# Kernel optimization log

Measured on AMD Instinct MI355X. Metric: run time of the kernel, lower is better.

Reference implementation:

```python
import jax, jax.numpy as jnp
import numpy as np

K, D = 512, 256

def setup_inputs() -> dict:
    key = jax.random.key(0)
    k1, k2 = jax.random.split(key)
    z_e = jax.random.normal(k1, (64, D, 32, 32), dtype=jnp.float32)
    # matches nn.Embedding weight init uniform_(-1/K, 1/K)
    codebook = jax.random.uniform(k2, (K, D), dtype=jnp.float32, minval=-1.0 / K, maxval=1.0 / K)
    return {"z_e": z_e, "codebook": codebook}

def reference(z_e, codebook):
    N, Dd, H, W = z_e.shape
    # NCHW -> (N*H*W, D) tokens
    x = jnp.transpose(z_e, (0, 2, 3, 1)).reshape(-1, Dd)
    x_sq = jnp.sum(x * x, axis=1, keepdims=True)            # [T, 1]
    w_sq = jnp.sum(codebook * codebook, axis=1)             # [K]
    dists = x_sq - 2.0 * (x @ codebook.T) + w_sq[None, :]   # [T, K]
    q = jnp.argmin(dists, axis=1)                           # [T]
    z_q = codebook[q]                                       # [T, D] gather
    z_q = z_q.reshape(N, H, W, Dd).transpose(0, 3, 1, 2)    # back to NCHW
    q = q.reshape(N, H, W).astype(jnp.int64)
    return (q, z_q)
```

## Files before the change

### kernel.cpp

```cpp
#include <hip/hip_runtime.h>
#include <float.h>
#include <math.h>


#define KCODES 512
#define DDIM   256
#define HWSZ   1024
#define TTOK   65536
#define TPB    64
#define NBLK   (TTOK / TPB)
#define NCHUNK 16
#define MARGIN 2.5e-4f

#define HW_OFF 66560
#define BK_OFF 68608
#define LDS_SZ 68864
#define ZQ_PITCH 1040

typedef short bf16x8 __attribute__((ext_vector_type(8)));
typedef float f32x16 __attribute__((ext_vector_type(16)));
typedef float f32x4  __attribute__((ext_vector_type(4)));

__device__ inline unsigned short bf16rne(float x) {
    union { float f; unsigned u; } a; a.f = x;
    unsigned r = a.u + (0x7fffu + ((a.u >> 16) & 1u));
    return (unsigned short)(r >> 16);
}
__device__ inline float bf16tof(unsigned short h) {
    union { unsigned u; float f; } b; b.u = ((unsigned)h) << 16; return b.f;
}

__device__ __forceinline__ void top4_insert(float m, int c, float fb[4], int fi[4]) {
    #pragma unroll
    for (int l = 0; l < 4; ++l) {
        const bool s = m > fb[l];
        const float nm = s ? fb[l] : m;
        const int   nc = s ? fi[l] : c;
        fb[l] = s ? m : fb[l];
        fi[l] = s ? c : fi[l];
        m = nm; c = nc;
    }
}

__global__ __launch_bounds__(256) void vq_wsq_np(const float* __restrict__ cb,
                                                 float* __restrict__ wsq) {
    const int tid = threadIdx.x;
    const int k = blockIdx.x * 16 + (tid >> 4);
    const int s = tid & 15, h2 = s >> 3, j2 = s & 7;
    const float* p = cb + (size_t)k * DDIM + h2 * 128 + j2;
    float v[16];
    #pragma unroll
    for (int i = 0; i < 16; ++i) v[i] = p[i * 8];
    float rr;
    {
#pragma clang fp contract(off)
        rr = v[0] * v[0];
        #pragma unroll
        for (int i = 1; i < 16; ++i) { float sq = v[i] * v[i]; rr = rr + sq; }
    }
    float t = rr;
    t = t + __shfl_xor(t, 1);
    t = t + __shfl_xor(t, 2);
    t = t + __shfl_xor(t, 4);
    t = t + __shfl_xor(t, 8);
    if (s == 0) wsq[k] = t;
}

__global__ __launch_bounds__(256) void vq_wpack(const float* __restrict__ cb,
                                                unsigned char* __restrict__ wsw) {
    const int gid = blockIdx.x * 256 + threadIdx.x;
    const int k = gid >> 5, o = gid & 31;
    const int d0 = o * 8, c = o >> 1, half = o & 1;
    unsigned hi[4], lo[4];
    #pragma unroll
    for (int jj = 0; jj < 4; ++jj) {
        float v0 = cb[k * DDIM + d0 + 2 * jj];
        float v1 = cb[k * DDIM + d0 + 2 * jj + 1];
        unsigned short h0 = bf16rne(v0), h1 = bf16rne(v1);
        unsigned short l0 = bf16rne(v0 - bf16tof(h0));
        unsigned short l1 = bf16rne(v1 - bf16tof(h1));
        hi[jj] = (unsigned)h0 | ((unsigned)h1 << 16);
        lo[jj] = (unsigned)l0 | ((unsigned)l1 << 16);
    }
    const int tile = k >> 5, lane2 = (k & 31) + 32 * half;
    *(uint4*)(wsw + ((size_t)((c * 2 + 0) * 16 + tile) * 1024) + lane2 * 16) = make_uint4(hi[0], hi[1], hi[2], hi[3]);
    *(uint4*)(wsw + ((size_t)((c * 2 + 1) * 16 + tile) * 1024) + lane2 * 16) = make_uint4(lo[0], lo[1], lo[2], lo[3]);
}

__global__ __launch_bounds__(512, 4) void vq_main(const float* __restrict__ z_e,
                                                  const float* __restrict__ cb,
                                                  const float* __restrict__ wsq,
                                                  const unsigned char* __restrict__ wsw,
                                                  float* __restrict__ out) {
    __shared__ __align__(16) unsigned char lds[LDS_SZ];

    const int tid = threadIdx.x;
    const int wv = tid >> 6, lane = tid & 63;
    const int tbase = blockIdx.x * TPB;
    const int n = tbase >> 10, hw0 = tbase & (HWSZ - 1);
    const float* zb = z_e + (size_t)n * (DDIM * HWSZ) + hw0;

    {
        const int tok = tid & 63, g = tid >> 6;
        const int mtS = tok >> 5;
        const int lbase = (tok & 31) * 16;
        #pragma unroll
        for (int o = 0; o < 4; ++o) {
            const int d0 = g * 32 + o * 8;
            float v[8];
            #pragma unroll
            for (int j = 0; j < 8; ++j) v[j] = zb[(size_t)(d0 + j) * HWSZ + tok];
            unsigned hi[4], lo[4];
            #pragma unroll
            for (int jj = 0; jj < 4; ++jj) {
                unsigned short h0 = bf16rne(v[2 * jj]), h1 = bf16rne(v[2 * jj + 1]);
                unsigned short l0 = bf16rne(v[2 * jj] - bf16tof(h0));
                unsigned short l1 = bf16rne(v[2 * jj + 1] - bf16tof(h1));
                hi[jj] = (unsigned)h0 | ((unsigned)h1 << 16);
                lo[jj] = (unsigned)l0 | ((unsigned)l1 << 16);
            }
            const int c = d0 >> 4;
            const int off2 = lbase + 512 * ((d0 >> 3) & 1);
            *(uint4*)(lds + ((0 * 2 + mtS) * 16 + c) * 1024 + off2) = make_uint4(hi[0], hi[1], hi[2], hi[3]);
            *(uint4*)(lds + ((1 * 2 + mtS) * 16 + c) * 1024 + off2) = make_uint4(lo[0], lo[1], lo[2], lo[3]);
        }
    }
    ((float*)(lds + HW_OFF))[tid] = 0.5f * wsq[tid];

    __syncthreads();

    const int qc = wv >> 1;
    const int mt = wv & 1;
    const int hh = lane >> 5;
    const float* hwsqL = (const float*)(lds + HW_OFF);

    #define LDW(c, p, t)   (*(const bf16x8*)(wsw + ((size_t)(((c) * 2 + (p)) * 16 + (t)) * 1024) + lane * 16))
    #define LDA(p, mm, c)  (*(const bf16x8*)(lds + (((p) * 2 + (mm)) * 16 + (c)) * 1024 + lane * 16))

    float fb[4] = {-FLT_MAX, -FLT_MAX, -FLT_MAX, -FLT_MAX};
    int   fi[4] = {KCODES, KCODES, KCODES, KCODES};

    #pragma unroll
    for (int pr = 0; pr < 2; ++pr) {
        const int ct0 = qc * 4 + 2 * pr;
        f32x16 a0, a1;
        #pragma unroll
        for (int r = 0; r < 16; ++r) { a0[r] = 0.f; a1[r] = 0.f; }
        bf16x8 Xc[2][2], Wc[2][4];
        Xc[0][0] = LDA(0, mt, 0);  Xc[0][1] = LDA(1, mt, 0);
        Wc[0][0] = LDW(0, 0, ct0); Wc[0][1] = LDW(0, 1, ct0);
        Wc[0][2] = LDW(0, 0, ct0 + 1); Wc[0][3] = LDW(0, 1, ct0 + 1);
        #pragma unroll
        for (int c = 0; c < NCHUNK; ++c) {
            const int cur = c & 1, nxt = cur ^ 1;
            if (c + 1 < NCHUNK) {
                Xc[nxt][0] = LDA(0, mt, c + 1);  Xc[nxt][1] = LDA(1, mt, c + 1);
                Wc[nxt][0] = LDW(c + 1, 0, ct0); Wc[nxt][1] = LDW(c + 1, 1, ct0);
                Wc[nxt][2] = LDW(c + 1, 0, ct0 + 1); Wc[nxt][3] = LDW(c + 1, 1, ct0 + 1);
            }
            a0 = __builtin_amdgcn_mfma_f32_32x32x16_bf16(Wc[cur][0], Xc[cur][0], a0, 0, 0, 0);
            a1 = __builtin_amdgcn_mfma_f32_32x32x16_bf16(Wc[cur][2], Xc[cur][0], a1, 0, 0, 0);
            a0 = __builtin_amdgcn_mfma_f32_32x32x16_bf16(Wc[cur][1], Xc[cur][0], a0, 0, 0, 0);
            a1 = __builtin_amdgcn_mfma_f32_32x32x16_bf16(Wc[cur][3], Xc[cur][0], a1, 0, 0, 0);
            a0 = __builtin_amdgcn_mfma_f32_32x32x16_bf16(Wc[cur][0], Xc[cur][1], a0, 0, 0, 0);
            a1 = __builtin_amdgcn_mfma_f32_32x32x16_bf16(Wc[cur][2], Xc[cur][1], a1, 0, 0, 0);
        }
        #pragma unroll
        for (int rq = 0; rq < 4; ++rq) {
            const f32x4 h40 = *(const f32x4*)(hwsqL + ct0 * 32 + rq * 8 + 4 * hh);
            const f32x4 h41 = *(const f32x4*)(hwsqL + (ct0 + 1) * 32 + rq * 8 + 4 * hh);
            #pragma unroll
            for (int rr = 0; rr < 4; ++rr) {
                top4_insert(a0[rq * 4 + rr] - h40[rr], ct0 * 32 + rr + 8 * rq + 4 * hh, fb, fi);
                top4_insert(a1[rq * 4 + rr] - h41[rr], (ct0 + 1) * 32 + rr + 8 * rq + 4 * hh, fb, fi);
            }
        }
    }

    {
        float sb[4]; int si[4];
        #pragma unroll
        for (int c = 0; c < 4; ++c) { sb[c] = __shfl_xor(fb[c], 32); si[c] = __shfl_xor(fi[c], 32); }
        #pragma unroll
        for (int c = 0; c < 4; ++c) top4_insert(sb[c], si[c], fb, fi);
    }

    __syncthreads();
    float* candm = (float*)lds;
    int*   candi = (int*)(lds + 4096);
    int*   wlCnt = (int*)(lds + 8192);
    int*   wlTok = (int*)(lds + 8208);
    int*   wlGi  = (int*)(lds + 8464);
    float* wlG   = (float*)(lds + 9488);
    int*   bkArr = (int*)(lds + BK_OFF);
    if (lane < 32) {
        const int slot = (qc * 64 + mt * 32 + lane) * 4;
        #pragma unroll
        for (int c = 0; c < 4; ++c) { candm[slot + c] = fb[c]; candi[slot + c] = fi[c]; }
    }
    if (tid == 0) *wlCnt = 0;
    __syncthreads();

    if (tid < TPB) {
        float g[4] = {-FLT_MAX, -FLT_MAX, -FLT_MAX, -FLT_MAX};
        int  gi[4] = {KCODES, KCODES, KCODES, KCODES};
        #pragma unroll
        for (int q4 = 0; q4 < 4; ++q4) {
            const int slot = (q4 * 64 + tid) * 4;
            #pragma unroll
            for (int c = 0; c < 4; ++c) top4_insert(candm[slot + c], candi[slot + c], g, gi);
        }
        if (g[0] - g[1] > MARGIN) {
            out[tbase + tid] = (float)gi[0];
            bkArr[tid] = gi[0];
        } else {
            const int slot = atomicAdd(wlCnt, 1);
            wlTok[slot] = tid;
            #pragma unroll
            for (int c = 0; c < 4; ++c) { wlGi[slot * 4 + c] = gi[c]; wlG[slot * 4 + c] = g[c]; }
        }
    }
    __syncthreads();

    {
        const int nIt = *wlCnt;
        for (int it = wv; it < nIt; it += 8) {
            const int tok = wlTok[it];
            const float g0 = wlG[it * 4];
            const float* xa = zb + tok;

            float xsq;
            {
                const int h2 = (lane >> 3) & 1, j2 = lane & 7;
                float v[16];
                if (lane < 16) {
                    #pragma unroll
                    for (int i = 0; i < 16; ++i)
                        v[i] = xa[(size_t)(h2 * 128 + i * 8 + j2) * HWSZ];
                } else {
                    #pragma unroll
                    for (int i = 0; i < 16; ++i) v[i] = 0.f;
                }
                float rr;
                {
#pragma clang fp contract(off)
                    rr = v[0] * v[0];
                    #pragma unroll
                    for (int i = 1; i < 16; ++i) { float sq = v[i] * v[i]; rr = rr + sq; }
                }
                float t = rr;
                t = t + __shfl_xor(t, 1);
                t = t + __shfl_xor(t, 2);
                t = t + __shfl_xor(t, 4);
                t = t + __shfl_xor(t, 8);
                xsq = __shfl(t, 0);
            }

            double xv[4];
            #pragma unroll
            for (int i = 0; i < 4; ++i)
                xv[i] = (double)xa[(size_t)(lane + 64 * i) * HWSZ];

            float bestd = FLT_MAX; int bestk = KCODES;
            #pragma unroll
            for (int c = 0; c < 4; ++c) {
                const float gc = wlG[it * 4 + c];
                if (c > 0 && g0 - gc > MARGIN) break;
                const int idx = wlGi[it * 4 + c];
                const float* wr = cb + (size_t)idx * DDIM;
                double A = 0.0;
                #pragma unroll
                for (int i = 0; i < 4; ++i)
                    A = fma((double)wr[lane + 64 * i], xv[i], A);
                A = A + __shfl_xor(A, 1);
                A = A + __shfl_xor(A, 2);
                A = A + __shfl_xor(A, 4);
                A = A + __shfl_xor(A, 8);
                A = A + __shfl_xor(A, 16);
                A = A + __shfl_xor(A, 32);
                float dist;
                {
#pragma clang fp contract(off)
                    const float xw = (float)A;
                    const float t1 = xsq - 2.0f * xw;
                    dist = t1 + wsq[idx];
                }
                if (dist < bestd || (dist == bestd && idx < bestk)) { bestd = dist; bestk = idx; }
            }
            if (lane == 0) {
                out[tbase + tok] = (float)bestk;
                bkArr[tok] = bestk;
            }
        }
    }
    __syncthreads();

    {
        #pragma unroll
        for (int rr = 0; rr < 8; ++rr) {
            const int r = wv * 8 + rr;
            const int bk = bkArr[r];
            const float4 vv = *(const float4*)(cb + (size_t)bk * DDIM + lane * 4);
            *(float4*)(lds + r * ZQ_PITCH + lane * 16) = vv;
        }
    }
    __syncthreads();

    {
        const int tk = tid & 63, s = tid >> 6;
        float* zq = out + TTOK + (size_t)n * (DDIM * HWSZ) + hw0 + tk;
        #pragma unroll
        for (int i = 0; i < 32; i += 4) {
            const f32x4 v = *(const f32x4*)(lds + tk * ZQ_PITCH + (s * 32 + i) * 4);
            #pragma unroll
            for (int j = 0; j < 4; ++j)
                zq[(size_t)(s * 32 + i + j) * HWSZ] = v[j];
        }
    }
}

extern "C" void kernel_launch(void* const* d_in, const int* in_sizes, int n_in,
                              void* d_out, int out_size, void* d_ws, size_t ws_size,
                              hipStream_t stream) {
    const float* z_e = (const float*)d_in[0];
    const float* cb  = (const float*)d_in[1];
    float* out = (float*)d_out;
    float* wsq = (float*)d_ws;
    unsigned char* wsw = (unsigned char*)d_ws + 2048;

    vq_wsq_np<<<32, 256, 0, stream>>>(cb, wsq);
    vq_wpack<<<64, 256, 0, stream>>>(cb, wsw);
    vq_main<<<NBLK, 512, 0, stream>>>(z_e, cb, wsq, wsw, out);
}
```

Before: 184.2 us.

## Halve tokens per block to 32 and merge codebook prep kernels

Each block in the main kernel now handles 32 tokens instead of 64, and each wave covers two code tiles for one token tile rather than four code tiles for two token tiles. This roughly halves LDS use per block, and launch bounds now request 8 blocks per CU to raise occupancy. The trade-off is less reuse of each codebook load from global memory, which roughly doubles codebook traffic. The two small prep kernels (squared norms and bf16 hi/lo packing) are fused into one launch to save a kernel launch.

```diff
diff --git a/kernel.cpp b/kernel.cpp
--- a/kernel.cpp
+++ b/kernel.cpp
@@ -7,14 +7,14 @@
 #define DDIM   256
 #define HWSZ   1024
 #define TTOK   65536
-#define TPB    64
+#define TPB    32
 #define NBLK   (TTOK / TPB)
 #define NCHUNK 16
 #define MARGIN 2.5e-4f
 
-#define HW_OFF 66560
-#define BK_OFF 68608
-#define LDS_SZ 68864
+#define HW_OFF 33280
+#define BK_OFF 35328
+#define LDS_SZ 35456
 #define ZQ_PITCH 1040
 
 typedef short bf16x8 __attribute__((ext_vector_type(8)));
@@ -42,52 +42,53 @@
     }
 }
 
-__global__ __launch_bounds__(256) void vq_wsq_np(const float* __restrict__ cb,
-                                                 float* __restrict__ wsq) {
+__global__ __launch_bounds__(256) void vq_prep(const float* __restrict__ cb,
+                                               unsigned char* __restrict__ wsw,
+                                               float* __restrict__ wsq) {
     const int tid = threadIdx.x;
-    const int k = blockIdx.x * 16 + (tid >> 4);
-    const int s = tid & 15, h2 = s >> 3, j2 = s & 7;
-    const float* p = cb + (size_t)k * DDIM + h2 * 128 + j2;
-    float v[16];
-    #pragma unroll
-    for (int i = 0; i < 16; ++i) v[i] = p[i * 8];
-    float rr;
-    {
+    const int gid = blockIdx.x * 256 + tid;
+    {
+        const int k = gid >> 5, o = gid & 31;
+        const int d0 = o * 8, c = o >> 1, half = o & 1;
+        unsigned hi[4], lo[4];
+        #pragma unroll
+        for (int jj = 0; jj < 4; ++jj) {
+            float v0 = cb[k * DDIM + d0 + 2 * jj];
+            float v1 = cb[k * DDIM + d0 + 2 * jj + 1];
+            unsigned short h0 = bf16rne(v0), h1 = bf16rne(v1);
+            unsigned short l0 = bf16rne(v0 - bf16tof(h0));
+            unsigned short l1 = bf16rne(v1 - bf16tof(h1));
+            hi[jj] = (unsigned)h0 | ((unsigned)h1 << 16);
+            lo[jj] = (unsigned)l0 | ((unsigned)l1 << 16);
+        }
+        const int tile = k >> 5, lane2 = (k & 31) + 32 * half;
+        *(uint4*)(wsw + ((size_t)((c * 2 + 0) * 16 + tile) * 1024) + lane2 * 16) = make_uint4(hi[0], hi[1], hi[2], hi[3]);
+        *(uint4*)(wsw + ((size_t)((c * 2 + 1) * 16 + tile) * 1024) + lane2 * 16) = make_uint4(lo[0], lo[1], lo[2], lo[3]);
+    }
+    if (blockIdx.x < 32) {
+        const int k = blockIdx.x * 16 + (tid >> 4);
+        const int s = tid & 15, h2 = s >> 3, j2 = s & 7;
+        const float* p = cb + (size_t)k * DDIM + h2 * 128 + j2;
+        float v[16];
+        #pragma unroll
+        for (int i = 0; i < 16; ++i) v[i] = p[i * 8];
+        float rr;
+        {
 #pragma clang fp contract(off)
-        rr = v[0] * v[0];
-        #pragma unroll
-        for (int i = 1; i < 16; ++i) { float sq = v[i] * v[i]; rr = rr + sq; }
-    }
-    float t = rr;
-    t = t + __shfl_xor(t, 1);
-    t = t + __shfl_xor(t, 2);
-    t = t + __shfl_xor(t, 4);
-    t = t + __shfl_xor(t, 8);
-    if (s == 0) wsq[k] = t;
-}
-
-__global__ __launch_bounds__(256) void vq_wpack(const float* __restrict__ cb,
-                                                unsigned char* __restrict__ wsw) {
-    const int gid = blockIdx.x * 256 + threadIdx.x;
-    const int k = gid >> 5, o = gid & 31;
-    const int d0 = o * 8, c = o >> 1, half = o & 1;
-    unsigned hi[4], lo[4];
-    #pragma unroll
-    for (int jj = 0; jj < 4; ++jj) {
-        float v0 = cb[k * DDIM + d0 + 2 * jj];
-        float v1 = cb[k * DDIM + d0 + 2 * jj + 1];
-        unsigned short h0 = bf16rne(v0), h1 = bf16rne(v1);
-        unsigned short l0 = bf16rne(v0 - bf16tof(h0));
-        unsigned short l1 = bf16rne(v1 - bf16tof(h1));
-        hi[jj] = (unsigned)h0 | ((unsigned)h1 << 16);
-        lo[jj] = (unsigned)l0 | ((unsigned)l1 << 16);
-    }
-    const int tile = k >> 5, lane2 = (k & 31) + 32 * half;
-    *(uint4*)(wsw + ((size_t)((c * 2 + 0) * 16 + tile) * 1024) + lane2 * 16) = make_uint4(hi[0], hi[1], hi[2], hi[3]);
-    *(uint4*)(wsw + ((size_t)((c * 2 + 1) * 16 + tile) * 1024) + lane2 * 16) = make_uint4(lo[0], lo[1], lo[2], lo[3]);
-}
-
-__global__ __launch_bounds__(512, 4) void vq_main(const float* __restrict__ z_e,
+            rr = v[0] * v[0];
+            #pragma unroll
+            for (int i = 1; i < 16; ++i) { float sq = v[i] * v[i]; rr = rr + sq; }
+        }
+        float t = rr;
+        t = t + __shfl_xor(t, 1);
+        t = t + __shfl_xor(t, 2);
+        t = t + __shfl_xor(t, 4);
+        t = t + __shfl_xor(t, 8);
+        if (s == 0) wsq[k] = t;
+    }
+}
+
+__global__ __launch_bounds__(512, 8) void vq_main(const float* __restrict__ z_e,
                                                   const float* __restrict__ cb,
                                                   const float* __restrict__ wsq,
                                                   const unsigned char* __restrict__ wsw,
@@ -101,12 +102,10 @@
     const float* zb = z_e + (size_t)n * (DDIM * HWSZ) + hw0;
 
     {
-        const int tok = tid & 63, g = tid >> 6;
-        const int mtS = tok >> 5;
-        const int lbase = (tok & 31) * 16;
-        #pragma unroll
-        for (int o = 0; o < 4; ++o) {
-            const int d0 = g * 32 + o * 8;
+        const int tok = tid & 31, g = (tid >> 5) & 15;
+        #pragma unroll
+        for (int o = 0; o < 2; ++o) {
+            const int d0 = g * 16 + o * 8;
             float v[8];
             #pragma unroll
             for (int j = 0; j < 8; ++j) v[j] = zb[(size_t)(d0 + j) * HWSZ + tok];
@@ -119,42 +118,38 @@
                 hi[jj] = (unsigned)h0 | ((unsigned)h1 << 16);
                 lo[jj] = (unsigned)l0 | ((unsigned)l1 << 16);
             }
-            const int c = d0 >> 4;
-            const int off2 = lbase + 512 * ((d0 >> 3) & 1);
-            *(uint4*)(lds + ((0 * 2 + mtS) * 16 + c) * 1024 + off2) = make_uint4(hi[0], hi[1], hi[2], hi[3]);
-            *(uint4*)(lds + ((1 * 2 + mtS) * 16 + c) * 1024 + off2) = make_uint4(lo[0], lo[1], lo[2], lo[3]);
+            const int off2 = tok * 16 + 512 * o;
+            *(uint4*)(lds + ((0 * 16 + g)) * 1024 + off2) = make_uint4(hi[0], hi[1], hi[2], hi[3]);
+            *(uint4*)(lds + ((1 * 16 + g)) * 1024 + off2) = make_uint4(lo[0], lo[1], lo[2], lo[3]);
         }
     }
     ((float*)(lds + HW_OFF))[tid] = 0.5f * wsq[tid];
 
     __syncthreads();
 
-    const int qc = wv >> 1;
-    const int mt = wv & 1;
     const int hh = lane >> 5;
+    const int ct0 = wv * 2;
     const float* hwsqL = (const float*)(lds + HW_OFF);
 
     #define LDW(c, p, t)   (*(const bf16x8*)(wsw + ((size_t)(((c) * 2 + (p)) * 16 + (t)) * 1024) + lane * 16))
-    #define LDA(p, mm, c)  (*(const bf16x8*)(lds + (((p) * 2 + (mm)) * 16 + (c)) * 1024 + lane * 16))
+    #define LDA(p, c)      (*(const bf16x8*)(lds + (((p) * 16 + (c))) * 1024 + lane * 16))
 
     float fb[4] = {-FLT_MAX, -FLT_MAX, -FLT_MAX, -FLT_MAX};
     int   fi[4] = {KCODES, KCODES, KCODES, KCODES};
 
-    #pragma unroll
-    for (int pr = 0; pr < 2; ++pr) {
-        const int ct0 = qc * 4 + 2 * pr;
+    {
         f32x16 a0, a1;
         #pragma unroll
         for (int r = 0; r < 16; ++r) { a0[r] = 0.f; a1[r] = 0.f; }
         bf16x8 Xc[2][2], Wc[2][4];
-        Xc[0][0] = LDA(0, mt, 0);  Xc[0][1] = LDA(1, mt, 0);
+        Xc[0][0] = LDA(0, 0);  Xc[0][1] = LDA(1, 0);
         Wc[0][0] = LDW(0, 0, ct0); Wc[0][1] = LDW(0, 1, ct0);
         Wc[0][2] = LDW(0, 0, ct0 + 1); Wc[0][3] = LDW(0, 1, ct0 + 1);
         #pragma unroll
         for (int c = 0; c < NCHUNK; ++c) {
             const int cur = c & 1, nxt = cur ^ 1;
             if (c + 1 < NCHUNK) {
-                Xc[nxt][0] = LDA(0, mt, c + 1);  Xc[nxt][1] = LDA(1, mt, c + 1);
+                Xc[nxt][0] = LDA(0, c + 1);  Xc[nxt][1] = LDA(1, c + 1);
                 Wc[nxt][0] = LDW(c + 1, 0, ct0); Wc[nxt][1] = LDW(c + 1, 1, ct0);
                 Wc[nxt][2] = LDW(c + 1, 0, ct0 + 1); Wc[nxt][3] = LDW(c + 1, 1, ct0 + 1);
             }
@@ -190,11 +185,11 @@
     int*   candi = (int*)(lds + 4096);
     int*   wlCnt = (int*)(lds + 8192);
     int*   wlTok = (int*)(lds + 8208);
-    int*   wlGi  = (int*)(lds + 8464);
-    float* wlG   = (float*)(lds + 9488);
+    int*   wlGi  = (int*)(lds + 8336);
+    float* wlG   = (float*)(lds + 8848);
     int*   bkArr = (int*)(lds + BK_OFF);
     if (lane < 32) {
-        const int slot = (qc * 64 + mt * 32 + lane) * 4;
+        const int slot = (wv * 32 + lane) * 4;
         #pragma unroll
         for (int c = 0; c < 4; ++c) { candm[slot + c] = fb[c]; candi[slot + c] = fi[c]; }
     }
@@ -205,8 +200,8 @@
         float g[4] = {-FLT_MAX, -FLT_MAX, -FLT_MAX, -FLT_MAX};
         int  gi[4] = {KCODES, KCODES, KCODES, KCODES};
         #pragma unroll
-        for (int q4 = 0; q4 < 4; ++q4) {
-            const int slot = (q4 * 64 + tid) * 4;
+        for (int w8 = 0; w8 < 8; ++w8) {
+            const int slot = (w8 * 32 + tid) * 4;
             #pragma unroll
             for (int c = 0; c < 4; ++c) top4_insert(candm[slot + c], candi[slot + c], g, gi);
         }
@@ -297,8 +292,8 @@
 
     {
         #pragma unroll
-        for (int rr = 0; rr < 8; ++rr) {
-            const int r = wv * 8 + rr;
+        for (int rr = 0; rr < 4; ++rr) {
+            const int r = wv * 4 + rr;
             const int bk = bkArr[r];
             const float4 vv = *(const float4*)(cb + (size_t)bk * DDIM + lane * 4);
             *(float4*)(lds + r * ZQ_PITCH + lane * 16) = vv;
@@ -307,14 +302,14 @@
     __syncthreads();
 
     {
-        const int tk = tid & 63, s = tid >> 6;
+        const int tk = tid & 31, s = tid >> 5;
         float* zq = out + TTOK + (size_t)n * (DDIM * HWSZ) + hw0 + tk;
         #pragma unroll
-        for (int i = 0; i < 32; i += 4) {
-            const f32x4 v = *(const f32x4*)(lds + tk * ZQ_PITCH + (s * 32 + i) * 4);
+        for (int i = 0; i < 16; i += 4) {
+            const f32x4 v = *(const f32x4*)(lds + tk * ZQ_PITCH + (s * 16 + i) * 4);
             #pragma unroll
             for (int j = 0; j < 4; ++j)
-                zq[(size_t)(s * 32 + i + j) * HWSZ] = v[j];
+                zq[(size_t)(s * 16 + i + j) * HWSZ] = v[j];
         }
     }
 }
@@ -328,7 +323,6 @@
     float* wsq = (float*)d_ws;
     unsigned char* wsw = (unsigned char*)d_ws + 2048;
 
-    vq_wsq_np<<<32, 256, 0, stream>>>(cb, wsq);
-    vq_wpack<<<64, 256, 0, stream>>>(cb, wsw);
+    vq_prep<<<64, 256, 0, stream>>>(cb, wsw, wsq);
     vq_main<<<NBLK, 512, 0, stream>>>(z_e, cb, wsq, wsw, out);
 }
```

New measurement: 227.8 us. 1.24x slower.
